# Optimization experiments

Measured on AMD Instinct MI355X. Metric: run time of the kernel, lower is better.

The kernel has to match this reference:

```python
import jax, jax.numpy as jnp
import numpy as np

SIG = 0.5  # radial Gaussian width of basis profiles

def _profiles(ksize, radii):
    c = (ksize - 1) // 2
    ys, xs = np.mgrid[-c:c + 1, -c:c + 1].astype(np.float32)
    rr = np.sqrt(ys ** 2 + xs ** 2)
    phi = np.arctan2(ys, xs)
    f = np.exp(-((rr[None] - np.asarray(radii, np.float32)[:, None, None]) ** 2) / (2 * SIG ** 2))
    f = f / f.sum(axis=(1, 2), keepdims=True)
    return f.astype(np.float32), phi.astype(np.float32)

def _steerable_basis():
    # create_radial(2) -> 5x5 kernels; k=0 uses radii {0,1,2}, k>=1 uses radii {1,2}
    f0, _ = _profiles(5, [0.0, 1.0, 2.0])          # [3,5,5]
    f, phi = _profiles(5, [1.0, 2.0])              # [2,5,5]
    Bc = np.stack([f * np.cos(k * phi) for k in (1, 2)])  # [2,2,5,5]
    Bs = np.stack([f * np.sin(k * phi) for k in (1, 2)])  # [2,2,5,5]
    return jnp.asarray(f0), jnp.asarray(Bc), jnp.asarray(Bs)

def _ortho_basis():
    # OrthoKernelBase.create_radial(3) -> 7x7 (cos phi, sin phi) vector kernels, radii {1,2,3}
    f, phi = _profiles(7, [1.0, 2.0, 3.0])
    return jnp.asarray(f * np.cos(phi)), jnp.asarray(f * np.sin(phi))

def _convT(x, k, stride=2):
    # torch conv_transpose2d(stride=2, padding='same') -> output H*stride
    return jax.lax.conv_transpose(x, k, strides=(stride, stride), padding='SAME',
                                  dimension_numbers=('NCHW', 'OIHW', 'NCHW'))

def setup_inputs() -> dict:
    key = jax.random.key(0)
    ks = jax.random.split(key, 6)
    B, Cin, Cout, H, W = 8, 64, 64, 64, 64
    x = jax.random.normal(ks[0], (B, Cin, H, W), jnp.float32)
    s = np.float32(1.0 / np.sqrt(Cin * 25))
    w0 = jax.random.normal(ks[1], (Cout, Cin, 3), jnp.float32) * s
    wc = jax.random.normal(ks[2], (2, Cout, Cin, 2), jnp.float32) * s
    ws = jax.random.normal(ks[3], (2, Cout, Cin, 2), jnp.float32) * s
    wa = jax.random.normal(ks[4], (Cout, Cin, 3), jnp.float32) * np.float32(1.0 / np.sqrt(Cin * 49))
    b = np.float32(1.0 / np.sqrt(Cout))
    bias = jax.random.uniform(ks[5], (Cout,), jnp.float32, minval=-b, maxval=b)
    return {"x": x, "w0": w0, "wc": wc, "ws": ws, "wa": wa, "bias": bias}

def reference(x, w0, wc, ws, wa, bias):
    B0, Bc, Bs = _steerable_basis()
    Ac, As = _ortho_basis()
    n_out = w0.shape[0]
    # --- attention: ortho conv-transpose producing a steering vector field (u,v)
    #     per output feature at the output resolution ---
    Ka = jnp.concatenate([jnp.einsum('oir,rhw->oihw', wa, Ac),
                          jnp.einsum('oir,rhw->oihw', wa, As)], axis=0)  # [2*n_out,n_in,7,7]
    uv = _convT(x, Ka)                      # [B, 2*n_out, 2H, 2W]
    u, v = uv[:, :n_out], uv[:, n_out:]
    # --- normalize_vector + tanh(rho) ---
    rho_raw = jnp.sqrt(u * u + v * v + 1e-8)
    un, vn = u / rho_raw, v / rho_raw        # unit steering vector (cos t, sin t)
    rho = jnp.tanh(rho_raw)
    c1, s1 = un, vn
    c2, s2 = un * un - vn * vn, 2.0 * un * vn   # Chebyshev: cos 2t, sin 2t
    # --- synthesize steerable kernels from basis and run one stacked conv-transpose ---
    K0 = jnp.einsum('oir,rhw->oihw', w0, B0)
    Kc = jnp.einsum('koir,krhw->koihw', wc, Bc)
    Ks = jnp.einsum('koir,krhw->koihw', ws, Bs)
    Kall = jnp.concatenate([K0, Kc[0], Ks[0], Kc[1], Ks[1]], axis=0)  # [5*n_out,n_in,5,5]
    y = _convT(x, Kall)                      # [B, 5*n_out, 2H, 2W]
    b_, _, Ho, Wo = y.shape
    y = y.reshape(b_, 5, n_out, Ho, Wo)
    out = y[:, 0] + rho * (c1 * y[:, 1] + s1 * y[:, 2] + c2 * y[:, 3] + s2 * y[:, 4])
    return out + bias[None, :, None, None]
```

## Files before the change

kernel.cpp:

```cpp
#include <hip/hip_runtime.h>
#include <math.h>


namespace {

typedef float f4 __attribute__((ext_vector_type(4)));
typedef short s8 __attribute__((ext_vector_type(8)));

constexpr int NKA = 401408;
constexpr int NKB = 512000;

__device__ __forceinline__ unsigned short f2bf(float f) {
    unsigned int u = __float_as_uint(f);
    u += 0x7fffu + ((u >> 16) & 1u);
    return (unsigned short)(u >> 16);
}

__global__ __launch_bounds__(256) void prep_kernel(
    const float* __restrict__ w0, const float* __restrict__ wc,
    const float* __restrict__ wsn, const float* __restrict__ wa,
    unsigned short* __restrict__ KA, unsigned short* __restrict__ KB,
    float sa0, float sa1, float sa2, float s50, float s51, float s52)
{
    const float SA[3] = {sa0, sa1, sa2};
    const float S5[3] = {s50, s51, s52};
    const int idx = blockIdx.x * 256 + threadIdx.x;
    if (idx < NKA) {
        int i = idx & 63;
        int e = idx >> 6;
        int oc = e & 63; e >>= 6;
        int uv = e & 1;  e >>= 1;
        int par = (e < 16) ? 0 : (e < 28) ? 1 : (e < 40) ? 2 : 3;
        int t = e - ((par == 0) ? 0 : (par == 1) ? 16 : (par == 2) ? 28 : 40);
        int py = par >> 1, px = par & 1;
        int nx = 4 - px;
        int tyi = t / nx, txi = t % nx;
        float dy = (float)(2 * tyi + py - 3), dx = (float)(2 * txi + px - 3);
        float rr = sqrtf(dy * dy + dx * dx);
        float phi = atan2f(dy, dx);
        const float* wr = wa + (oc * 64 + i) * 3;
        float v = 0.f;
#pragma unroll
        for (int r = 0; r < 3; ++r) { float d = rr - (float)(r + 1); v += wr[r] * (expf(-2.f * d * d) / SA[r]); }
        float tr = uv ? sinf(phi) : cosf(phi);
        KA[idx] = f2bf(v * tr);
    } else if (idx < NKA + NKB) {
        int j = idx - NKA;
        int i = j & 63;
        int rest = j >> 6;
        int oc = rest % 320;
        int e = rest / 320;
        int par = (e < 4) ? 0 : (e < 10) ? 1 : (e < 16) ? 2 : 3;
        int t = e - ((par == 0) ? 0 : (par == 1) ? 4 : (par == 2) ? 10 : 16);
        int py = par >> 1, px = par & 1;
        int nx = 2 + px;
        int tyi = t / nx, txi = t % nx;
        float dy = (float)(2 * tyi - 1 - py), dx = (float)(2 * txi - 1 - px);
        float rr = sqrtf(dy * dy + dx * dx);
        float phi = atan2f(dy, dx);
        int g = oc >> 6, o = oc & 63;
        float v = 0.f;
        if (g == 0) {
            const float* wr = w0 + (o * 64 + i) * 3;
#pragma unroll
            for (int r = 0; r < 3; ++r) { float d = rr - (float)r; v += wr[r] * (expf(-2.f * d * d) / S5[r]); }
        } else {
            int k = (g - 1) >> 1, sn = (g - 1) & 1;
            const float* wsel = ((sn == 0) ? wc : wsn) + ((k * 64 + o) * 64 + i) * 2;
            float s = 0.f;
#pragma unroll
            for (int r = 0; r < 2; ++r) { float d = rr - (float)(r + 1); s += wsel[r] * (expf(-2.f * d * d) / S5[r + 1]); }
            float ang = (float)(k + 1) * phi;
            v = s * ((sn == 0) ? cosf(ang) : sinf(ang));
        }
        KB[j] = f2bf(v);
    }
}

__global__ __launch_bounds__(256) void transpose_kernel(
    const float* __restrict__ x, unsigned short* __restrict__ Xt)
{
    __shared__ float LF[64][65];
    const int t = threadIdx.x;
    const int iyp = blockIdx.x, b = blockIdx.y;
    const int iy = iyp - 2;
    unsigned int* Xtu = (unsigned int*)(Xt + (size_t)(b * 68 + iyp) * 68 * 64);
    if (iy < 0 || iy >= 64) {
        for (int k = t; k < 68 * 32; k += 256) Xtu[k] = 0u;
        return;
    }
    const float* xb = x + (size_t)b * 262144 + iy * 64;
#pragma unroll
    for (int it = 0; it < 16; ++it) {
        int ch = it * 4 + (t >> 6);
        LF[ch][t & 63] = xb[(size_t)ch * 4096 + (t & 63)];
    }
    __syncthreads();
    if (t < 128) {
        int colidx = t >> 5;
        int ixp = (colidx < 2) ? colidx : 64 + colidx;
        Xtu[ixp * 32 + (t & 31)] = 0u;
    }
    const int lane = t & 63, w = t >> 6;
#pragma unroll
    for (int k = 0; k < 8; ++k) {
        int it = w * 8 + k;
        int ix = 2 * it + (lane >> 5);
        int ch = 2 * (lane & 31);
        unsigned int pack = (unsigned int)f2bf(LF[ch][ix]) | ((unsigned int)f2bf(LF[ch + 1][ix]) << 16);
        Xtu[(ix + 2) * 32 + (lane & 31)] = pack;
    }
}

template <int PY, int PX>
__device__ __forceinline__ void mfma_loop(
    const unsigned short* __restrict__ Xs,
    const unsigned short* __restrict__ KA, const unsigned short* __restrict__ KB,
    const float* __restrict__ bias, float* __restrict__ out,
    int b, int oy, int obase, int lr, int hi)
{
    constexpr int NXA = 4 - PX, NYA = 4 - PY, NTA = NYA * NXA;
    constexpr int NXB = 2 + PX, NYB = 2 + PY;
    constexpr int PAR = 2 * PY + PX;
    constexpr int TBA = (PAR == 0) ? 0 : (PAR == 1) ? 16 : (PAR == 2) ? 28 : 40;
    constexpr int TBB = (PAR == 0) ? 0 : (PAR == 1) ? 4  : (PAR == 2) ? 10 : 16;

    f4 accA[2][4];
    f4 accB[5][4];
#pragma unroll
    for (int uv = 0; uv < 2; ++uv)
#pragma unroll
        for (int ni = 0; ni < 4; ++ni) accA[uv][ni] = f4{0.f, 0.f, 0.f, 0.f};
#pragma unroll
    for (int g = 0; g < 5; ++g)
#pragma unroll
        for (int ni = 0; ni < 4; ++ni) accB[g][ni] = f4{0.f, 0.f, 0.f, 0.f};

#pragma unroll
    for (int tA = 0; tA < NTA; ++tA) {
        const int tyi = tA / NXA, txi = tA % NXA;
        const int tyiB = tyi - (1 - PY), txiB = txi - (1 - PX);
        const bool bval = (tyiB >= 0) && (tyiB < NYB) && (txiB >= 0) && (txiB < NXB);
#pragma unroll
        for (int ks = 0; ks < 2; ++ks) {
            s8 bfr[4];
#pragma unroll
            for (int ni = 0; ni < 4; ++ni) {
                const int rx = ni * 16 + lr + txi + PX;
                const int gz = (ks * 4 + hi) ^ (rx & 7);
                bfr[ni] = *(const s8*)(Xs + ((tyi * 68 + rx) * 8 + gz) * 8);
            }
            {
                s8 aA[2];
#pragma unroll
                for (int uv = 0; uv < 2; ++uv)
                    aA[uv] = *(const s8*)(KA + (((TBA + tA) * 2 + uv) * 64 + obase + lr) * 64 + ks * 32 + hi * 8);
#pragma unroll
                for (int uv = 0; uv < 2; ++uv)
#pragma unroll
                    for (int ni = 0; ni < 4; ++ni)
                        accA[uv][ni] = __builtin_amdgcn_mfma_f32_16x16x32_bf16(aA[uv], bfr[ni], accA[uv][ni], 0, 0, 0);
            }
            if (bval) {
                const int tB = tyiB * NXB + txiB;
                s8 aB[5];
#pragma unroll
                for (int g = 0; g < 5; ++g)
                    aB[g] = *(const s8*)(KB + ((TBB + tB) * 320 + g * 64 + obase + lr) * 64 + ks * 32 + hi * 8);
#pragma unroll
                for (int g = 0; g < 5; ++g)
#pragma unroll
                    for (int ni = 0; ni < 4; ++ni)
                        accB[g][ni] = __builtin_amdgcn_mfma_f32_16x16x32_bf16(aB[g], bfr[ni], accB[g][ni], 0, 0, 0);
            }
        }
    }

    const int yy = 2 * oy + PY;
#pragma unroll
    for (int ni = 0; ni < 4; ++ni) {
        const int px = ni * 16 + lr;
        const int xx = 2 * px + PX;
#pragma unroll
        for (int r2 = 0; r2 < 4; ++r2) {
            const int o = obase + hi * 4 + r2;
            const float u = accA[0][ni][r2], v = accA[1][ni][r2];
            const float rho_raw = sqrtf(u * u + v * v + 1e-8f);
            const float un = u / rho_raw, vn = v / rho_raw;
            const float rho = tanhf(rho_raw);
            const float c2 = (un - vn) * (un + vn);
            const float sp = 2.f * un * vn;
            out[((b * 64 + o) * 128 + yy) * 128 + xx] =
                accB[0][ni][r2]
                + rho * (un * accB[1][ni][r2] + vn * accB[2][ni][r2]
                       + c2 * accB[3][ni][r2] + sp * accB[4][ni][r2])
                + bias[o];
        }
    }
}

template <int PY>
__device__ __forceinline__ void fused_body(
    const unsigned short* __restrict__ Xt,
    const unsigned short* __restrict__ KA, const unsigned short* __restrict__ KB,
    const float* __restrict__ bias, float* __restrict__ out,
    int oh, unsigned short* Xs)
{
    constexpr int NYA = 4 - PY;
    const int tid = threadIdx.x;
    const int oy = blockIdx.x, b = blockIdx.y;

    {
        const int iy0 = oy - (2 - PY);
        const unsigned short* XtB = Xt + (size_t)b * 68 * 68 * 64;
        const int ngr = NYA * 68 * 8;
        for (int g = tid; g < ngr; g += 256) {
            const int row = g / 544;
            const int rem = g - row * 544;
            const int rx = rem >> 3, gz = rem & 7;
            const int iyp = iy0 + row + 2;
            const s8 v = *(const s8*)(XtB + (((iyp * 68 + rx) * 8) + (gz ^ (rx & 7))) * 8);
            *(s8*)(Xs + ((row * 68 + rx) * 8 + gz) * 8) = v;
        }
    }
    __syncthreads();

    const int lane = tid & 63, lr = lane & 15, hi = lane >> 4;
    const int w = tid >> 6;
    const int p = w & 1, mq = w >> 1;
    const int obase = oh * 32 + mq * 16;

    if (p == 0)
        mfma_loop<PY, 0>(Xs, KA, KB, bias, out, b, oy, obase, lr, hi);
    else
        mfma_loop<PY, 1>(Xs, KA, KB, bias, out, b, oy, obase, lr, hi);
}

__global__ __launch_bounds__(256, 2) void fused_kernel(
    const unsigned short* __restrict__ Xt,
    const unsigned short* __restrict__ KA, const unsigned short* __restrict__ KB,
    const float* __restrict__ bias, float* __restrict__ out)
{
    __shared__ __align__(16) unsigned short Xs[4 * 68 * 64];
    const int z = blockIdx.z;
    const int oh = z >> 1;
    if (z & 1) fused_body<1>(Xt, KA, KB, bias, out, oh, Xs);
    else       fused_body<0>(Xt, KA, KB, bias, out, oh, Xs);
}

}

extern "C" void kernel_launch(void* const* d_in, const int* in_sizes, int n_in,
                              void* d_out, int out_size, void* d_ws, size_t ws_size,
                              hipStream_t stream)
{
    const float* x    = (const float*)d_in[0];
    const float* w0   = (const float*)d_in[1];
    const float* wc   = (const float*)d_in[2];
    const float* wsn  = (const float*)d_in[3];
    const float* wa   = (const float*)d_in[4];
    const float* bias = (const float*)d_in[5];
    float* out = (float*)d_out;

    char* wsb = (char*)d_ws;
    unsigned short* KA = (unsigned short*)(wsb);
    unsigned short* KB = (unsigned short*)(wsb + 802816);
    unsigned short* Xt = (unsigned short*)(wsb + 2097152);

    float SA[3] = {0.f, 0.f, 0.f}, S5[3] = {0.f, 0.f, 0.f};
    for (int ky = 0; ky < 7; ++ky)
        for (int kx = 0; kx < 7; ++kx) {
            float dy = (float)(ky - 3), dx = (float)(kx - 3);
            float rr = sqrtf(dy * dy + dx * dx);
            for (int r = 0; r < 3; ++r) { float d = rr - (float)(r + 1); SA[r] += expf(-2.f * d * d); }
        }
    for (int ky = 0; ky < 5; ++ky)
        for (int kx = 0; kx < 5; ++kx) {
            float dy = (float)(ky - 2), dx = (float)(kx - 2);
            float rr = sqrtf(dy * dy + dx * dx);
            for (int r = 0; r < 3; ++r) { float d = rr - (float)r; S5[r] += expf(-2.f * d * d); }
        }

    prep_kernel<<<dim3(3568), dim3(256), 0, stream>>>(w0, wc, wsn, wa, KA, KB,
                                                      SA[0], SA[1], SA[2], S5[0], S5[1], S5[2]);
    transpose_kernel<<<dim3(68, 8), dim3(256), 0, stream>>>(x, Xt);
    fused_kernel<<<dim3(64, 8, 4), dim3(256), 0, stream>>>(Xt, KA, KB, bias, out);
}
```

Before: 235.3 us.

## Merge prep/transpose launches, prefetch-pipeline MFMA loop, use direct global-to-LDS loads

Merges the weight-prep and input-transpose kernels into one launch by splitting on block index, which removes one kernel launch. The transpose now writes the swizzled layout directly, so the fused kernel can copy its input rows into shared memory with global_load_lds instead of staging through registers. The MFMA loop is software-pipelined, loading the next k-slice's weights and input fragments while the current one computes. Validity of the B taps is precomputed as a compile-time bitmask. The cost is higher register pressure from the double-buffered fragments.

```diff
diff --git a/kernel.cpp b/kernel.cpp
--- a/kernel.cpp
+++ b/kernel.cpp
@@ -16,14 +16,24 @@
     return (unsigned short)(u >> 16);
 }
 
-__global__ __launch_bounds__(256) void prep_kernel(
+template <int PY, int PX>
+constexpr unsigned bmaskA() {
+    constexpr int NXA = 4 - PX, NYA = 4 - PY, NXB = 2 + PX, NYB = 2 + PY;
+    unsigned m = 0;
+    for (int t = 0; t < NYA * NXA; ++t) {
+        int tyi = t / NXA, txi = t % NXA;
+        int ty = tyi - (1 - PY), tx = txi - (1 - PX);
+        if (ty >= 0 && ty < NYB && tx >= 0 && tx < NXB) m |= 1u << t;
+    }
+    return m;
+}
+
+__device__ void prep_body(
     const float* __restrict__ w0, const float* __restrict__ wc,
     const float* __restrict__ wsn, const float* __restrict__ wa,
     unsigned short* __restrict__ KA, unsigned short* __restrict__ KB,
-    float sa0, float sa1, float sa2, float s50, float s51, float s52)
-{
-    const float SA[3] = {sa0, sa1, sa2};
-    const float S5[3] = {s50, s51, s52};
+    const float* SA, const float* S5)
+{
     const int idx = blockIdx.x * 256 + threadIdx.x;
     if (idx < NKA) {
         int i = idx & 63;
@@ -77,12 +87,13 @@
     }
 }
 
-__global__ __launch_bounds__(256) void transpose_kernel(
-    const float* __restrict__ x, unsigned short* __restrict__ Xt)
-{
-    __shared__ float LF[64][65];
+__device__ void transpose_body(
+    const float* __restrict__ x, unsigned short* __restrict__ Xt, float* LFraw)
+{
+    float (*LF)[65] = (float (*)[65])LFraw;
     const int t = threadIdx.x;
-    const int iyp = blockIdx.x, b = blockIdx.y;
+    const int j = blockIdx.x - 3568;
+    const int iyp = j % 68, b = j / 68;
     const int iy = iyp - 2;
     unsigned int* Xtu = (unsigned int*)(Xt + (size_t)(b * 68 + iyp) * 68 * 64);
     if (iy < 0 || iy >= 64) {
@@ -108,8 +119,25 @@
         int ix = 2 * it + (lane >> 5);
         int ch = 2 * (lane & 31);
         unsigned int pack = (unsigned int)f2bf(LF[ch][ix]) | ((unsigned int)f2bf(LF[ch + 1][ix]) << 16);
-        Xtu[(ix + 2) * 32 + (lane & 31)] = pack;
-    }
+        const int ixp = ix + 2;
+        const int gslot = ((lane & 31) >> 2) ^ (ixp & 7);
+        Xtu[ixp * 32 + gslot * 4 + ((lane & 31) & 3)] = pack;
+    }
+}
+
+__global__ __launch_bounds__(256) void setup_kernel(
+    const float* __restrict__ w0, const float* __restrict__ wc,
+    const float* __restrict__ wsn, const float* __restrict__ wa,
+    const float* __restrict__ x,
+    unsigned short* __restrict__ KA, unsigned short* __restrict__ KB,
+    unsigned short* __restrict__ Xt,
+    float sa0, float sa1, float sa2, float s50, float s51, float s52)
+{
+    __shared__ float LFraw[64 * 65];
+    const float SA[3] = {sa0, sa1, sa2};
+    const float S5[3] = {s50, s51, s52};
+    if (blockIdx.x < 3568) prep_body(w0, wc, wsn, wa, KA, KB, SA, S5);
+    else                   transpose_body(x, Xt, LFraw);
 }
 
 template <int PY, int PX>
@@ -120,10 +148,13 @@
     int b, int oy, int obase, int lr, int hi)
 {
     constexpr int NXA = 4 - PX, NYA = 4 - PY, NTA = NYA * NXA;
-    constexpr int NXB = 2 + PX, NYB = 2 + PY;
     constexpr int PAR = 2 * PY + PX;
     constexpr int TBA = (PAR == 0) ? 0 : (PAR == 1) ? 16 : (PAR == 2) ? 28 : 40;
     constexpr int TBB = (PAR == 0) ? 0 : (PAR == 1) ? 4  : (PAR == 2) ? 10 : 16;
+    constexpr unsigned BM = bmaskA<PY, PX>();
+
+    const unsigned short* ka = KA + TBA * 8192  + (obase + lr) * 64 + hi * 8;
+    const unsigned short* kb = KB + TBB * 20480 + (obase + lr) * 64 + hi * 8;
 
     f4 accA[2][4];
     f4 accB[5][4];
@@ -136,44 +167,64 @@
 #pragma unroll
         for (int ni = 0; ni < 4; ++ni) accB[g][ni] = f4{0.f, 0.f, 0.f, 0.f};
 
-#pragma unroll
-    for (int tA = 0; tA < NTA; ++tA) {
-        const int tyi = tA / NXA, txi = tA % NXA;
-        const int tyiB = tyi - (1 - PY), txiB = txi - (1 - PX);
-        const bool bval = (tyiB >= 0) && (tyiB < NYB) && (txiB >= 0) && (txiB < NXB);
-#pragma unroll
-        for (int ks = 0; ks < 2; ++ks) {
-            s8 bfr[4];
-#pragma unroll
-            for (int ni = 0; ni < 4; ++ni) {
-                const int rx = ni * 16 + lr + txi + PX;
-                const int gz = (ks * 4 + hi) ^ (rx & 7);
-                bfr[ni] = *(const s8*)(Xs + ((tyi * 68 + rx) * 8 + gz) * 8);
-            }
-            {
-                s8 aA[2];
-#pragma unroll
-                for (int uv = 0; uv < 2; ++uv)
-                    aA[uv] = *(const s8*)(KA + (((TBA + tA) * 2 + uv) * 64 + obase + lr) * 64 + ks * 32 + hi * 8);
-#pragma unroll
-                for (int uv = 0; uv < 2; ++uv)
-#pragma unroll
-                    for (int ni = 0; ni < 4; ++ni)
-                        accA[uv][ni] = __builtin_amdgcn_mfma_f32_16x16x32_bf16(aA[uv], bfr[ni], accA[uv][ni], 0, 0, 0);
-            }
-            if (bval) {
-                const int tB = tyiB * NXB + txiB;
-                s8 aB[5];
-#pragma unroll
-                for (int g = 0; g < 5; ++g)
-                    aB[g] = *(const s8*)(KB + ((TBB + tB) * 320 + g * 64 + obase + lr) * 64 + ks * 32 + hi * 8);
-#pragma unroll
-                for (int g = 0; g < 5; ++g)
-#pragma unroll
-                    for (int ni = 0; ni < 4; ++ni)
-                        accB[g][ni] = __builtin_amdgcn_mfma_f32_16x16x32_bf16(aB[g], bfr[ni], accB[g][ni], 0, 0, 0);
-            }
-        }
+    s8 a0[2], a1[2], g0[5], g1[5], x0[4], x1[4];
+
+    auto loadA = [&](s8 (&d)[2], int t, int ks) {
+#pragma unroll
+        for (int uv = 0; uv < 2; ++uv)
+            d[uv] = *(const s8*)(ka + t * 8192 + uv * 4096 + ks * 32);
+    };
+    auto loadG = [&](s8 (&d)[5], int tB, int ks) {
+#pragma unroll
+        for (int g = 0; g < 5; ++g)
+            d[g] = *(const s8*)(kb + tB * 20480 + g * 4096 + ks * 32);
+    };
+    auto loadX = [&](s8 (&d)[4], int tyi, int txi, int ks) {
+#pragma unroll
+        for (int ni = 0; ni < 4; ++ni) {
+            const int rx = ni * 16 + lr + txi + PX;
+            const int gz = (ks * 4 + hi) ^ (rx & 7);
+            d[ni] = *(const s8*)(Xs + ((tyi * 68 + rx) * 8 + gz) * 8);
+        }
+    };
+    auto mmA = [&](s8 (&a)[2], s8 (&xx)[4]) {
+#pragma unroll
+        for (int uv = 0; uv < 2; ++uv)
+#pragma unroll
+            for (int ni = 0; ni < 4; ++ni)
+                accA[uv][ni] = __builtin_amdgcn_mfma_f32_16x16x32_bf16(a[uv], xx[ni], accA[uv][ni], 0, 0, 0);
+    };
+    auto mmB = [&](s8 (&gg)[5], s8 (&xx)[4]) {
+#pragma unroll
+        for (int g = 0; g < 5; ++g)
+#pragma unroll
+            for (int ni = 0; ni < 4; ++ni)
+                accB[g][ni] = __builtin_amdgcn_mfma_f32_16x16x32_bf16(gg[g], xx[ni], accB[g][ni], 0, 0, 0);
+    };
+
+    loadA(a0, 0, 0);
+    loadX(x0, 0, 0, 0);
+    if (BM & 1u) loadG(g0, 0, 0);
+
+    int tyi = 0, txi = 0, tB = 0;
+#pragma unroll
+    for (int t = 0; t < NTA; ++t) {
+        const bool bv = (BM >> t) & 1u;
+        loadA(a1, t, 1);
+        loadX(x1, tyi, txi, 1);
+        if (bv) loadG(g1, tB, 1);
+        mmA(a0, x0);
+        if (bv) mmB(g0, x0);
+        const int txn = (txi + 1 == NXA) ? 0 : txi + 1;
+        const int tyn = (txi + 1 == NXA) ? tyi + 1 : tyi;
+        if (t + 1 < NTA) {
+            loadA(a0, t + 1, 0);
+            loadX(x0, tyn, txn, 0);
+            if ((BM >> (t + 1)) & 1u) loadG(g0, tB + (bv ? 1 : 0), 0);
+        }
+        mmA(a1, x1);
+        if (bv) { mmB(g1, x1); ++tB; }
+        tyi = tyn; txi = txn;
     }
 
     const int yy = 2 * oy + PY;
@@ -211,17 +262,14 @@
     const int oy = blockIdx.x, b = blockIdx.y;
 
     {
-        const int iy0 = oy - (2 - PY);
-        const unsigned short* XtB = Xt + (size_t)b * 68 * 68 * 64;
-        const int ngr = NYA * 68 * 8;
-        for (int g = tid; g < ngr; g += 256) {
-            const int row = g / 544;
-            const int rem = g - row * 544;
-            const int rx = rem >> 3, gz = rem & 7;
-            const int iyp = iy0 + row + 2;
-            const s8 v = *(const s8*)(XtB + (((iyp * 68 + rx) * 8) + (gz ^ (rx & 7))) * 8);
-            *(s8*)(Xs + ((row * 68 + rx) * 8 + gz) * 8) = v;
-        }
+        const int iy0p = oy + PY;
+        const int lane = tid & 63;
+        const unsigned short* src = Xt + ((size_t)b * 68 + iy0p) * 68 * 64;
+        constexpr int NCH = (NYA * 68 * 8 + 63) / 64;
+        const int wv = tid >> 6;
+        for (int c = wv; c < NCH; c += 4)
+            __builtin_amdgcn_global_load_lds((const unsigned int*)(src + c * 512 + lane * 8),
+                                             (unsigned int*)(Xs + c * 512), 16, 0, 0);
     }
     __syncthreads();
 
@@ -281,8 +329,9 @@
             for (int r = 0; r < 3; ++r) { float d = rr - (float)r; S5[r] += expf(-2.f * d * d); }
         }
 
-    prep_kernel<<<dim3(3568), dim3(256), 0, stream>>>(w0, wc, wsn, wa, KA, KB,
-                                                      SA[0], SA[1], SA[2], S5[0], S5[1], S5[2]);
-    transpose_kernel<<<dim3(68, 8), dim3(256), 0, stream>>>(x, Xt);
+    setup_kernel<<<dim3(3568 + 544), dim3(256), 0, stream>>>(
+        w0, wc, wsn, wa, x, KA, KB, Xt,
+        SA[0], SA[1], SA[2], S5[0], S5[1], S5[2]);
+
     fused_kernel<<<dim3(64, 8, 4), dim3(256), 0, stream>>>(Xt, KA, KB, bias, out);
 }
```

Result: no change. 238.1 us (+1.2%).
